# Kernel optimization log

Hardware: AMD Instinct MI355X
Metric: run time of the kernel (lower is better)

## Reference

```python
import jax, jax.numpy as jnp
import numpy as np

N_NODES = 1_000_000
E = 262_144
N_FEAT_COLS = 9        # columns 1..9 of x
CARD = 50_000          # cardinality of each feature embedding table
EMB = 128
EDGE_DIM = 27
# node type (col 0) that activates each feature column h (h = col index - 1):
# files (type 0) use cols 1..4, processes (type 1) use col 5, sockets (type 2) use cols 6..9
TYPE_PER_COL = (0, 0, 0, 0, 1, 2, 2, 2, 2)


def setup_inputs() -> dict:
    key = jax.random.key(0)
    ks = jax.random.split(key, 10)
    type_col = jax.random.randint(ks[0], (N_NODES, 1), 0, 3, dtype=jnp.int32)
    feat_cols = jax.random.randint(ks[1], (N_NODES, N_FEAT_COLS), 0, CARD, dtype=jnp.int32)
    x = jnp.concatenate([type_col, feat_cols], axis=1)  # [N_NODES, 10]
    src = jax.random.randint(ks[2], (E,), 0, N_NODES, dtype=jnp.int32)
    dst = jax.random.randint(ks[3], (E,), 0, N_NODES, dtype=jnp.int32)
    neg_dst = jax.random.randint(ks[4], (E,), 0, N_NODES, dtype=jnp.int32)
    msg = jax.random.normal(ks[5], (E, EDGE_DIM), dtype=jnp.float32)
    emb_type = jax.random.normal(ks[6], (3, EMB), dtype=jnp.float32)            # embeddings[0]
    emb_feats = jax.random.normal(ks[7], (N_FEAT_COLS, CARD, EMB), dtype=jnp.float32)  # embeddings[1..9]
    edge_w = jax.random.normal(ks[8], (EMB, EDGE_DIM), dtype=jnp.float32) / np.sqrt(EDGE_DIM)
    edge_b = jnp.zeros((EMB,), dtype=jnp.float32)
    out_w = jax.random.normal(ks[9], (1, EMB), dtype=jnp.float32) / np.sqrt(EMB)
    out_b = jnp.zeros((1,), dtype=jnp.float32)
    return dict(x=x, src=src, dst=dst, neg_dst=neg_dst, msg=msg,
                emb_type=emb_type, emb_feats=emb_feats,
                edge_w=edge_w, edge_b=edge_b, out_w=out_w, out_b=out_b)


def _encode_features(rows, emb_type, emb_feats):
    """rows: [E,10] int. Equivalent to torch encode_features: per node type,
    sum the type-specific embedding lookups; col-0 (type) embedding is shared."""
    t = rows[:, 0]                     # [E] node type
    out = emb_type[t]                  # embeddings[0] applies to every type
    for h in range(N_FEAT_COLS):       # small fixed loop over 9 tables
        mask = (t == TYPE_PER_COL[h]).astype(out.dtype)[:, None]   # [E,1]
        out = out + emb_feats[h][rows[:, h + 1]] * mask            # masked gather-sum
    return out                         # [E, EMB]


def reference(x, src, dst, neg_dst, msg, emb_type, emb_feats, edge_w, edge_b, out_w, out_b):
    h_src = _encode_features(x[src], emb_type, emb_feats)       # [E, EMB]
    h_pos_dst = _encode_features(x[dst], emb_type, emb_feats)
    h_neg_dst = _encode_features(x[neg_dst], emb_type, emb_feats)
    target_msg = msg @ edge_w.T + edge_b                        # Linear(edge_dim -> EMB)
    h_pos_edge = jax.nn.relu(h_src + h_pos_dst)
    h_neg_edge = jax.nn.relu(h_src + h_neg_dst)
    pos = (h_pos_edge + target_msg) @ out_w.T + out_b           # [E, 1]
    neg = (h_neg_edge + target_msg) @ out_w.T + out_b           # [E, 1]
    return (pos, neg)
```

## Files before the change

### kernel.cpp

```cpp
#include <hip/hip_runtime.h>
#include <hip/hip_fp16.h>

#define N_NODES 1000000
#define NUM_EDGES 262144
#define CARD 50000
#define EMB 128
#define EDGE_DIM 27

typedef float vfloat4 __attribute__((ext_vector_type(4)));
typedef unsigned int vuint4 __attribute__((ext_vector_type(4)));

#define XPACK_OFF 4096
#define EMB16_OFF (XPACK_OFF + (size_t)N_NODES * 16)
#define EMB_ELEMS (9ull * CARD * EMB)
#define WS_NEEDED (EMB16_OFF + EMB_ELEMS * 2)

__global__ void prep_kernel(const float* __restrict__ edge_w,
                            const float* __restrict__ edge_b,
                            const float* __restrict__ out_w,
                            const float* __restrict__ out_b,
                            float* __restrict__ ws) {
    int j = threadIdx.x;
    if (j < EDGE_DIM) {
        float s = 0.f;
        for (int k = 0; k < EMB; ++k) s += out_w[k] * edge_w[k * EDGE_DIM + j];
        ws[j] = s;
    } else if (j == EDGE_DIM) {
        float s = out_b[0];
        for (int k = 0; k < EMB; ++k) s += edge_b[k] * out_w[k];
        ws[EDGE_DIM] = s;
    }
}

__global__ __launch_bounds__(256) void pack_x_kernel(const int* __restrict__ x,
                                                     uint4* __restrict__ xp) {
    int i = blockIdx.x * 256 + threadIdx.x;
    if (i >= N_NODES) return;
    const int* r = x + (size_t)i * 10;
    const int t  = __builtin_nontemporal_load(r + 0);
    const int c1 = __builtin_nontemporal_load(r + 1);
    const int c2 = __builtin_nontemporal_load(r + 2);
    const int c3 = __builtin_nontemporal_load(r + 3);
    const int c4 = __builtin_nontemporal_load(r + 4);
    const int c5 = __builtin_nontemporal_load(r + 5);
    const int c6 = __builtin_nontemporal_load(r + 6);
    const int c7 = __builtin_nontemporal_load(r + 7);
    const int c8 = __builtin_nontemporal_load(r + 8);
    const int c9 = __builtin_nontemporal_load(r + 9);
    unsigned i0, i1, i2, i3, pad = 0;
    if (t == 0) {
        i0 = (unsigned)c1;
        i1 = 1u * CARD + (unsigned)c2;
        i2 = 2u * CARD + (unsigned)c3;
        i3 = 3u * CARD + (unsigned)c4;
    } else if (t == 1) {
        i0 = i1 = i2 = i3 = 4u * CARD + (unsigned)c5;
        pad = 1u;
    } else {
        i0 = 5u * CARD + (unsigned)c6;
        i1 = 6u * CARD + (unsigned)c7;
        i2 = 7u * CARD + (unsigned)c8;
        i3 = 8u * CARD + (unsigned)c9;
    }
    uint4 o;
    o.x = i0 | ((unsigned)t << 20) | (pad << 22);
    o.y = i1;
    o.z = i2;
    o.w = i3;
    xp[i] = o;
}

__global__ __launch_bounds__(256) void cvt_emb_kernel(const float* __restrict__ src,
                                                      __half* __restrict__ dst) {
    size_t i = ((size_t)blockIdx.x * 256 + threadIdx.x) * 8;
    vfloat4 a = __builtin_nontemporal_load((const vfloat4*)(src + i));
    vfloat4 b = __builtin_nontemporal_load((const vfloat4*)(src + i + 4));
    __half2 h0 = __floats2half2_rn(a.x, a.y);
    __half2 h1 = __floats2half2_rn(a.z, a.w);
    __half2 h2 = __floats2half2_rn(b.x, b.y);
    __half2 h3 = __floats2half2_rn(b.z, b.w);
    vuint4 o;
    o.x = *(unsigned*)&h0;
    o.y = *(unsigned*)&h1;
    o.z = *(unsigned*)&h2;
    o.w = *(unsigned*)&h3;
    *(vuint4*)(dst + i) = o;
}

__global__ __launch_bounds__(256, 4) void edge_pred_fp16(
    const uint4* __restrict__ xp, const int* __restrict__ src,
    const int* __restrict__ dst, const int* __restrict__ neg_dst,
    const float* __restrict__ msg, const float* __restrict__ emb_type,
    const __half* __restrict__ e16, const float* __restrict__ out_w,
    const float* __restrict__ ws, float* __restrict__ out) {
    const int lane = threadIdx.x & 63;
    const int wave = threadIdx.x >> 6;
    const int e0 = __builtin_amdgcn_readfirstlane(blockIdx.x * 8 + wave * 2);

    const int half = lane >> 5;
    const int hl = lane & 31;
    const int loff = lane * 2;

    int nodes[6];
    nodes[0] = src[e0];     nodes[1] = dst[e0];     nodes[2] = neg_dst[e0];
    nodes[3] = src[e0 + 1]; nodes[4] = dst[e0 + 1]; nodes[5] = neg_dst[e0 + 1];

    float mterm = 0.f;
    if (hl < EDGE_DIM) {
        mterm = __builtin_nontemporal_load(msg + (size_t)(e0 + half) * EDGE_DIM + hl) * ws[hl];
    }

    float2 v0[6];
    unsigned u[6][4];
    float wpad[6];
#pragma unroll
    for (int n = 0; n < 6; ++n) {
        const uint4 px = xp[nodes[n]];
        const unsigned t = (px.x >> 20) & 3u;
        wpad[n] = (px.x & (1u << 22)) ? 0.f : 1.f;
        const size_t i0 = (size_t)(px.x & 0xFFFFFu);

        v0[n] = *(const float2*)(emb_type + (size_t)t * EMB + loff);
        u[n][0] = *(const unsigned*)((const char*)e16 + (i0 * EMB + loff) * 2);
        u[n][1] = *(const unsigned*)((const char*)e16 + ((size_t)px.y * EMB + loff) * 2);
        u[n][2] = *(const unsigned*)((const char*)e16 + ((size_t)px.z * EMB + loff) * 2);
        u[n][3] = *(const unsigned*)((const char*)e16 + ((size_t)px.w * EMB + loff) * 2);
    }
    const float2 wv = *(const float2*)(out_w + loff);

    __builtin_amdgcn_sched_barrier(0);

    float hx[6], hy[6];
#pragma unroll
    for (int n = 0; n < 6; ++n) {
        const float2 f1 = __half22float2(*(const __half2*)&u[n][0]);
        const float2 f2 = __half22float2(*(const __half2*)&u[n][1]);
        const float2 f3 = __half22float2(*(const __half2*)&u[n][2]);
        const float2 f4 = __half22float2(*(const __half2*)&u[n][3]);
        const float ax = v0[n].x + f1.x;
        const float ay = v0[n].y + f1.y;
        const float bx = f2.x + f3.x + f4.x;
        const float by = f2.y + f3.y + f4.y;
        hx[n] = ax + wpad[n] * bx;
        hy[n] = ay + wpad[n] * by;
    }

    float p0 = fmaxf(hx[0] + hx[1], 0.f) * wv.x + fmaxf(hy[0] + hy[1], 0.f) * wv.y;
    float q0 = fmaxf(hx[0] + hx[2], 0.f) * wv.x + fmaxf(hy[0] + hy[2], 0.f) * wv.y;
    float p1 = fmaxf(hx[3] + hx[4], 0.f) * wv.x + fmaxf(hy[3] + hy[4], 0.f) * wv.y;
    float q1 = fmaxf(hx[3] + hx[5], 0.f) * wv.x + fmaxf(hy[3] + hy[5], 0.f) * wv.y;

    if (half == 0) { p0 += mterm; q0 += mterm; }
    else           { p1 += mterm; q1 += mterm; }

    p0 += __shfl_xor(p0, 32, 64);
    q0 += __shfl_xor(q0, 32, 64);
    p1 += __shfl_xor(p1, 32, 64);
    q1 += __shfl_xor(q1, 32, 64);
    float pz = half ? p1 : p0;
    float qz = half ? q1 : q0;
#pragma unroll
    for (int off = 16; off > 0; off >>= 1) {
        pz += __shfl_xor(pz, off, 64);
        qz += __shfl_xor(qz, off, 64);
    }

    if (hl == 0) {
        const float b2 = ws[EDGE_DIM];
        const int e = e0 + half;
        out[e] = pz + b2;
        out[NUM_EDGES + e] = qz + b2;
    }
}

__global__ __launch_bounds__(256, 4) void edge_pred_kernel(
    const int* __restrict__ x, const int* __restrict__ src,
    const int* __restrict__ dst, const int* __restrict__ neg_dst,
    const float* __restrict__ msg, const float* __restrict__ emb_type,
    const float* __restrict__ emb_feats, const float* __restrict__ out_w,
    const float* __restrict__ ws, float* __restrict__ out) {
    const int lane = threadIdx.x & 63;
    const int wave = threadIdx.x >> 6;
    const int e0 = __builtin_amdgcn_readfirstlane(blockIdx.x * 8 + wave * 2);

    const int half = lane >> 5;
    const int hl = lane & 31;
    const int loff = lane * 2;

    int nodes[6];
    nodes[0] = src[e0];     nodes[1] = dst[e0];     nodes[2] = neg_dst[e0];
    nodes[3] = src[e0 + 1]; nodes[4] = dst[e0 + 1]; nodes[5] = neg_dst[e0 + 1];

    float mterm = 0.f;
    if (hl < EDGE_DIM) {
        mterm = __builtin_nontemporal_load(msg + (size_t)(e0 + half) * EDGE_DIM + hl) * ws[hl];
    }

    float2 v[6][5];
    float wpad[6];
#pragma unroll
    for (int n = 0; n < 6; ++n) {
        const int* xr = x + (size_t)nodes[n] * 10;
        const int t = xr[0];
        const int c1 = xr[1], c2 = xr[2], c3 = xr[3], c4 = xr[4], c5 = xr[5],
                  c6 = xr[6], c7 = xr[7], c8 = xr[8], c9 = xr[9];
        const int i0 = (t == 0) ? c1 : (t == 1) ? c5 : c6;
        const int i1 = (t == 0) ? c2 : (t == 1) ? c5 : c7;
        const int i2 = (t == 0) ? c3 : (t == 1) ? c5 : c8;
        const int i3 = (t == 0) ? c4 : (t == 1) ? c5 : c9;
        const int h0 = (t == 0) ? 0 : (t == 1) ? 4 : 5;
        const int h1 = (t == 0) ? 1 : (t == 1) ? 4 : 6;
        const int h2 = (t == 0) ? 2 : (t == 1) ? 4 : 7;
        const int h3 = (t == 0) ? 3 : (t == 1) ? 4 : 8;
        wpad[n] = (t == 1) ? 0.f : 1.f;

        v[n][0] = *(const float2*)(emb_type + (size_t)t * EMB + loff);
        v[n][1] = *(const float2*)(emb_feats + ((size_t)h0 * CARD + (size_t)i0) * EMB + loff);
        v[n][2] = *(const float2*)(emb_feats + ((size_t)h1 * CARD + (size_t)i1) * EMB + loff);
        v[n][3] = *(const float2*)(emb_feats + ((size_t)h2 * CARD + (size_t)i2) * EMB + loff);
        v[n][4] = *(const float2*)(emb_feats + ((size_t)h3 * CARD + (size_t)i3) * EMB + loff);
    }
    const float2 wv = *(const float2*)(out_w + loff);

    __builtin_amdgcn_sched_barrier(0);

    float hx[6], hy[6];
#pragma unroll
    for (int n = 0; n < 6; ++n) {
        const float ax = v[n][0].x + v[n][1].x;
        const float ay = v[n][0].y + v[n][1].y;
        const float bx = v[n][2].x + v[n][3].x + v[n][4].x;
        const float by = v[n][2].y + v[n][3].y + v[n][4].y;
        hx[n] = ax + wpad[n] * bx;
        hy[n] = ay + wpad[n] * by;
    }

    float p0 = fmaxf(hx[0] + hx[1], 0.f) * wv.x + fmaxf(hy[0] + hy[1], 0.f) * wv.y;
    float q0 = fmaxf(hx[0] + hx[2], 0.f) * wv.x + fmaxf(hy[0] + hy[2], 0.f) * wv.y;
    float p1 = fmaxf(hx[3] + hx[4], 0.f) * wv.x + fmaxf(hy[3] + hy[4], 0.f) * wv.y;
    float q1 = fmaxf(hx[3] + hx[5], 0.f) * wv.x + fmaxf(hy[3] + hy[5], 0.f) * wv.y;

    if (half == 0) { p0 += mterm; q0 += mterm; }
    else           { p1 += mterm; q1 += mterm; }

    p0 += __shfl_xor(p0, 32, 64);
    q0 += __shfl_xor(q0, 32, 64);
    p1 += __shfl_xor(p1, 32, 64);
    q1 += __shfl_xor(q1, 32, 64);
    float pz = half ? p1 : p0;
    float qz = half ? q1 : q0;
#pragma unroll
    for (int off = 16; off > 0; off >>= 1) {
        pz += __shfl_xor(pz, off, 64);
        qz += __shfl_xor(qz, off, 64);
    }

    if (hl == 0) {
        const float b2 = ws[EDGE_DIM];
        const int e = e0 + half;
        out[e] = pz + b2;
        out[NUM_EDGES + e] = qz + b2;
    }
}

extern "C" void kernel_launch(void* const* d_in, const int* in_sizes, int n_in,
                              void* d_out, int out_size, void* d_ws, size_t ws_size,
                              hipStream_t stream) {
    const int* x = (const int*)d_in[0];
    const int* src = (const int*)d_in[1];
    const int* dst = (const int*)d_in[2];
    const int* neg_dst = (const int*)d_in[3];
    const float* msg = (const float*)d_in[4];
    const float* emb_type = (const float*)d_in[5];
    const float* emb_feats = (const float*)d_in[6];
    const float* edge_w = (const float*)d_in[7];
    const float* edge_b = (const float*)d_in[8];
    const float* out_w = (const float*)d_in[9];
    const float* out_b = (const float*)d_in[10];
    float* out = (float*)d_out;
    float* ws = (float*)d_ws;

    prep_kernel<<<1, 64, 0, stream>>>(edge_w, edge_b, out_w, out_b, ws);

    const int blocks = NUM_EDGES / 8;

    if (ws_size >= WS_NEEDED) {
        uint4* xp = (uint4*)((char*)d_ws + XPACK_OFF);
        __half* e16 = (__half*)((char*)d_ws + EMB16_OFF);
        pack_x_kernel<<<(N_NODES + 255) / 256, 256, 0, stream>>>(x, xp);
        cvt_emb_kernel<<<28125, 256, 0, stream>>>(emb_feats, e16);
        edge_pred_fp16<<<blocks, 256, 0, stream>>>(xp, src, dst, neg_dst, msg,
                                                   emb_type, e16, out_w, ws, out);
    } else {
        edge_pred_kernel<<<blocks, 256, 0, stream>>>(x, src, dst, neg_dst, msg,
                                                     emb_type, emb_feats, out_w,
                                                     ws, out);
    }
}
```

Baseline: 473.9 us.

## Merge prep kernels into one launch and process four edges per wave

The separate pack_x and fp16 conversion kernels become a single launch that dispatches on block index, removing one launch and the gap between them. The fp16 edge kernel now handles four edges per wave instead of two, with 12 node gathers in flight per lane and a quarter-wave reduction. This raises memory-level parallelism per wave and halves the grid, at the cost of more registers per thread and possibly lower occupancy.

```diff
diff --git a/kernel.cpp b/kernel.cpp
--- a/kernel.cpp
+++ b/kernel.cpp
@@ -14,6 +14,9 @@
 #define EMB16_OFF (XPACK_OFF + (size_t)N_NODES * 16)
 #define EMB_ELEMS (9ull * CARD * EMB)
 #define WS_NEEDED (EMB16_OFF + EMB_ELEMS * 2)
+
+#define CVT_BLOCKS 28125
+#define PACK_BLOCKS ((N_NODES + 255) / 256)
 
 __global__ void prep_kernel(const float* __restrict__ edge_w,
                             const float* __restrict__ edge_b,
@@ -32,59 +35,59 @@
     }
 }
 
-__global__ __launch_bounds__(256) void pack_x_kernel(const int* __restrict__ x,
-                                                     uint4* __restrict__ xp) {
-    int i = blockIdx.x * 256 + threadIdx.x;
-    if (i >= N_NODES) return;
-    const int* r = x + (size_t)i * 10;
-    const int t  = __builtin_nontemporal_load(r + 0);
-    const int c1 = __builtin_nontemporal_load(r + 1);
-    const int c2 = __builtin_nontemporal_load(r + 2);
-    const int c3 = __builtin_nontemporal_load(r + 3);
-    const int c4 = __builtin_nontemporal_load(r + 4);
-    const int c5 = __builtin_nontemporal_load(r + 5);
-    const int c6 = __builtin_nontemporal_load(r + 6);
-    const int c7 = __builtin_nontemporal_load(r + 7);
-    const int c8 = __builtin_nontemporal_load(r + 8);
-    const int c9 = __builtin_nontemporal_load(r + 9);
-    unsigned i0, i1, i2, i3, pad = 0;
-    if (t == 0) {
-        i0 = (unsigned)c1;
-        i1 = 1u * CARD + (unsigned)c2;
-        i2 = 2u * CARD + (unsigned)c3;
-        i3 = 3u * CARD + (unsigned)c4;
-    } else if (t == 1) {
-        i0 = i1 = i2 = i3 = 4u * CARD + (unsigned)c5;
-        pad = 1u;
+__global__ __launch_bounds__(256) void prep_stream_kernel(
+    const float* __restrict__ embf, __half* __restrict__ dst,
+    const int* __restrict__ x, uint4* __restrict__ xp) {
+    if (blockIdx.x < CVT_BLOCKS) {
+        size_t i = ((size_t)blockIdx.x * 256 + threadIdx.x) * 8;
+        vfloat4 a = __builtin_nontemporal_load((const vfloat4*)(embf + i));
+        vfloat4 b = __builtin_nontemporal_load((const vfloat4*)(embf + i + 4));
+        __half2 h0 = __floats2half2_rn(a.x, a.y);
+        __half2 h1 = __floats2half2_rn(a.z, a.w);
+        __half2 h2 = __floats2half2_rn(b.x, b.y);
+        __half2 h3 = __floats2half2_rn(b.z, b.w);
+        vuint4 o;
+        o.x = *(unsigned*)&h0;
+        o.y = *(unsigned*)&h1;
+        o.z = *(unsigned*)&h2;
+        o.w = *(unsigned*)&h3;
+        *(vuint4*)(dst + i) = o;
     } else {
-        i0 = 5u * CARD + (unsigned)c6;
-        i1 = 6u * CARD + (unsigned)c7;
-        i2 = 7u * CARD + (unsigned)c8;
-        i3 = 8u * CARD + (unsigned)c9;
-    }
-    uint4 o;
-    o.x = i0 | ((unsigned)t << 20) | (pad << 22);
-    o.y = i1;
-    o.z = i2;
-    o.w = i3;
-    xp[i] = o;
-}
-
-__global__ __launch_bounds__(256) void cvt_emb_kernel(const float* __restrict__ src,
-                                                      __half* __restrict__ dst) {
-    size_t i = ((size_t)blockIdx.x * 256 + threadIdx.x) * 8;
-    vfloat4 a = __builtin_nontemporal_load((const vfloat4*)(src + i));
-    vfloat4 b = __builtin_nontemporal_load((const vfloat4*)(src + i + 4));
-    __half2 h0 = __floats2half2_rn(a.x, a.y);
-    __half2 h1 = __floats2half2_rn(a.z, a.w);
-    __half2 h2 = __floats2half2_rn(b.x, b.y);
-    __half2 h3 = __floats2half2_rn(b.z, b.w);
-    vuint4 o;
-    o.x = *(unsigned*)&h0;
-    o.y = *(unsigned*)&h1;
-    o.z = *(unsigned*)&h2;
-    o.w = *(unsigned*)&h3;
-    *(vuint4*)(dst + i) = o;
+        int i = (blockIdx.x - CVT_BLOCKS) * 256 + threadIdx.x;
+        if (i >= N_NODES) return;
+        const int* r = x + (size_t)i * 10;
+        const int t  = __builtin_nontemporal_load(r + 0);
+        const int c1 = __builtin_nontemporal_load(r + 1);
+        const int c2 = __builtin_nontemporal_load(r + 2);
+        const int c3 = __builtin_nontemporal_load(r + 3);
+        const int c4 = __builtin_nontemporal_load(r + 4);
+        const int c5 = __builtin_nontemporal_load(r + 5);
+        const int c6 = __builtin_nontemporal_load(r + 6);
+        const int c7 = __builtin_nontemporal_load(r + 7);
+        const int c8 = __builtin_nontemporal_load(r + 8);
+        const int c9 = __builtin_nontemporal_load(r + 9);
+        unsigned i0, i1, i2, i3, pad = 0;
+        if (t == 0) {
+            i0 = (unsigned)c1;
+            i1 = 1u * CARD + (unsigned)c2;
+            i2 = 2u * CARD + (unsigned)c3;
+            i3 = 3u * CARD + (unsigned)c4;
+        } else if (t == 1) {
+            i0 = i1 = i2 = i3 = 4u * CARD + (unsigned)c5;
+            pad = 1u;
+        } else {
+            i0 = 5u * CARD + (unsigned)c6;
+            i1 = 6u * CARD + (unsigned)c7;
+            i2 = 7u * CARD + (unsigned)c8;
+            i3 = 8u * CARD + (unsigned)c9;
+        }
+        uint4 o;
+        o.x = i0 | ((unsigned)t << 20) | (pad << 22);
+        o.y = i1;
+        o.z = i2;
+        o.w = i3;
+        xp[i] = o;
+    }
 }
 
 __global__ __launch_bounds__(256, 4) void edge_pred_fp16(
@@ -95,26 +98,34 @@
     const float* __restrict__ ws, float* __restrict__ out) {
     const int lane = threadIdx.x & 63;
     const int wave = threadIdx.x >> 6;
-    const int e0 = __builtin_amdgcn_readfirstlane(blockIdx.x * 8 + wave * 2);
-
-    const int half = lane >> 5;
-    const int hl = lane & 31;
+    const int e0 = __builtin_amdgcn_readfirstlane(blockIdx.x * 16 + wave * 4);
+
+    const int q = lane >> 4;
+    const int ql = lane & 15;
     const int loff = lane * 2;
 
-    int nodes[6];
-    nodes[0] = src[e0];     nodes[1] = dst[e0];     nodes[2] = neg_dst[e0];
-    nodes[3] = src[e0 + 1]; nodes[4] = dst[e0 + 1]; nodes[5] = neg_dst[e0 + 1];
-
-    float mterm = 0.f;
-    if (hl < EDGE_DIM) {
-        mterm = __builtin_nontemporal_load(msg + (size_t)(e0 + half) * EDGE_DIM + hl) * ws[hl];
-    }
-
-    float2 v0[6];
-    unsigned u[6][4];
-    float wpad[6];
-#pragma unroll
-    for (int n = 0; n < 6; ++n) {
+    int nodes[12];
+#pragma unroll
+    for (int k = 0; k < 4; ++k) {
+        nodes[3 * k + 0] = src[e0 + k];
+        nodes[3 * k + 1] = dst[e0 + k];
+        nodes[3 * k + 2] = neg_dst[e0 + k];
+    }
+
+    float mterm;
+    {
+        const float* mrow = msg + (size_t)(e0 + q) * EDGE_DIM;
+        mterm = __builtin_nontemporal_load(mrow + ql) * ws[ql];
+        if (ql < EDGE_DIM - 16) {
+            mterm += __builtin_nontemporal_load(mrow + 16 + ql) * ws[16 + ql];
+        }
+    }
+
+    float2 v0[12];
+    unsigned u[12][4];
+    float wpad[12];
+#pragma unroll
+    for (int n = 0; n < 12; ++n) {
         const uint4 px = xp[nodes[n]];
         const unsigned t = (px.x >> 20) & 3u;
         wpad[n] = (px.x & (1u << 22)) ? 0.f : 1.f;
@@ -130,9 +141,9 @@
 
     __builtin_amdgcn_sched_barrier(0);
 
-    float hx[6], hy[6];
-#pragma unroll
-    for (int n = 0; n < 6; ++n) {
+    float hx[12], hy[12];
+#pragma unroll
+    for (int n = 0; n < 12; ++n) {
         const float2 f1 = __half22float2(*(const __half2*)&u[n][0]);
         const float2 f2 = __half22float2(*(const __half2*)&u[n][1]);
         const float2 f3 = __half22float2(*(const __half2*)&u[n][2]);
@@ -145,31 +156,45 @@
         hy[n] = ay + wpad[n] * by;
     }
 
-    float p0 = fmaxf(hx[0] + hx[1], 0.f) * wv.x + fmaxf(hy[0] + hy[1], 0.f) * wv.y;
-    float q0 = fmaxf(hx[0] + hx[2], 0.f) * wv.x + fmaxf(hy[0] + hy[2], 0.f) * wv.y;
-    float p1 = fmaxf(hx[3] + hx[4], 0.f) * wv.x + fmaxf(hy[3] + hy[4], 0.f) * wv.y;
-    float q1 = fmaxf(hx[3] + hx[5], 0.f) * wv.x + fmaxf(hy[3] + hy[5], 0.f) * wv.y;
-
-    if (half == 0) { p0 += mterm; q0 += mterm; }
-    else           { p1 += mterm; q1 += mterm; }
-
-    p0 += __shfl_xor(p0, 32, 64);
-    q0 += __shfl_xor(q0, 32, 64);
-    p1 += __shfl_xor(p1, 32, 64);
-    q1 += __shfl_xor(q1, 32, 64);
-    float pz = half ? p1 : p0;
-    float qz = half ? q1 : q0;
-#pragma unroll
-    for (int off = 16; off > 0; off >>= 1) {
-        pz += __shfl_xor(pz, off, 64);
-        qz += __shfl_xor(qz, off, 64);
-    }
-
-    if (hl == 0) {
+    float p0, p1, p2, p3, q0, q1, q2, q3;
+    {
+        p0 = fmaxf(hx[0] + hx[1], 0.f) * wv.x + fmaxf(hy[0] + hy[1], 0.f) * wv.y;
+        q0 = fmaxf(hx[0] + hx[2], 0.f) * wv.x + fmaxf(hy[0] + hy[2], 0.f) * wv.y;
+        p1 = fmaxf(hx[3] + hx[4], 0.f) * wv.x + fmaxf(hy[3] + hy[4], 0.f) * wv.y;
+        q1 = fmaxf(hx[3] + hx[5], 0.f) * wv.x + fmaxf(hy[3] + hy[5], 0.f) * wv.y;
+        p2 = fmaxf(hx[6] + hx[7], 0.f) * wv.x + fmaxf(hy[6] + hy[7], 0.f) * wv.y;
+        q2 = fmaxf(hx[6] + hx[8], 0.f) * wv.x + fmaxf(hy[6] + hy[8], 0.f) * wv.y;
+        p3 = fmaxf(hx[9] + hx[10], 0.f) * wv.x + fmaxf(hy[9] + hy[10], 0.f) * wv.y;
+        q3 = fmaxf(hx[9] + hx[11], 0.f) * wv.x + fmaxf(hy[9] + hy[11], 0.f) * wv.y;
+    }
+
+    if (q == 0) { p0 += mterm; q0 += mterm; }
+    else if (q == 1) { p1 += mterm; q1 += mterm; }
+    else if (q == 2) { p2 += mterm; q2 += mterm; }
+    else             { p3 += mterm; q3 += mterm; }
+
+    p0 += __shfl_xor(p0, 32, 64); p0 += __shfl_xor(p0, 16, 64);
+    q0 += __shfl_xor(q0, 32, 64); q0 += __shfl_xor(q0, 16, 64);
+    p1 += __shfl_xor(p1, 32, 64); p1 += __shfl_xor(p1, 16, 64);
+    q1 += __shfl_xor(q1, 32, 64); q1 += __shfl_xor(q1, 16, 64);
+    p2 += __shfl_xor(p2, 32, 64); p2 += __shfl_xor(p2, 16, 64);
+    q2 += __shfl_xor(q2, 32, 64); q2 += __shfl_xor(q2, 16, 64);
+    p3 += __shfl_xor(p3, 32, 64); p3 += __shfl_xor(p3, 16, 64);
+    q3 += __shfl_xor(q3, 32, 64); q3 += __shfl_xor(q3, 16, 64);
+
+    float zp = (q == 0) ? p0 : (q == 1) ? p1 : (q == 2) ? p2 : p3;
+    float zq = (q == 0) ? q0 : (q == 1) ? q1 : (q == 2) ? q2 : q3;
+#pragma unroll
+    for (int off = 8; off > 0; off >>= 1) {
+        zp += __shfl_xor(zp, off, 64);
+        zq += __shfl_xor(zq, off, 64);
+    }
+
+    if (ql == 0) {
         const float b2 = ws[EDGE_DIM];
-        const int e = e0 + half;
-        out[e] = pz + b2;
-        out[NUM_EDGES + e] = qz + b2;
+        const int e = e0 + q;
+        out[e] = zp + b2;
+        out[NUM_EDGES + e] = zq + b2;
     }
 }
 
@@ -282,16 +307,16 @@
 
     prep_kernel<<<1, 64, 0, stream>>>(edge_w, edge_b, out_w, out_b, ws);
 
-    const int blocks = NUM_EDGES / 8;
-
     if (ws_size >= WS_NEEDED) {
         uint4* xp = (uint4*)((char*)d_ws + XPACK_OFF);
         __half* e16 = (__half*)((char*)d_ws + EMB16_OFF);
-        pack_x_kernel<<<(N_NODES + 255) / 256, 256, 0, stream>>>(x, xp);
-        cvt_emb_kernel<<<28125, 256, 0, stream>>>(emb_feats, e16);
+        prep_stream_kernel<<<CVT_BLOCKS + PACK_BLOCKS, 256, 0, stream>>>(
+            emb_feats, e16, x, xp);
+        const int blocks = NUM_EDGES / 16;
         edge_pred_fp16<<<blocks, 256, 0, stream>>>(xp, src, dst, neg_dst, msg,
                                                    emb_type, e16, out_w, ws, out);
     } else {
+        const int blocks = NUM_EDGES / 8;
         edge_pred_kernel<<<blocks, 256, 0, stream>>>(x, src, dst, neg_dst, msg,
                                                      emb_type, emb_feats, out_w,
                                                      ws, out);
```

Result: slower. 484.9 us (+2.3%).

## Merge prep kernels into one streaming launch and precompute per-edge message term

Applied to the files above, without the earlier changes.

Combines the embedding fp16 conversion and node-index packing into a single kernel launch, partitioned by block index. A third block range computes the per-edge message dot product into a workspace array. The main gather kernel then reads one precomputed float per edge instead of loading msg rows, and writes outputs with nontemporal stores. This removes one launch boundary and takes the strided msg loads off the gather kernel, at the cost of an extra small workspace array and a dependency on ws from prep_kernel.

```diff
diff --git a/kernel.cpp b/kernel.cpp
--- a/kernel.cpp
+++ b/kernel.cpp
@@ -10,10 +10,15 @@
 typedef float vfloat4 __attribute__((ext_vector_type(4)));
 typedef unsigned int vuint4 __attribute__((ext_vector_type(4)));
 
-#define XPACK_OFF 4096
+#define MTERM_OFF 4096
+#define XPACK_OFF (MTERM_OFF + (size_t)NUM_EDGES * 4)
 #define EMB16_OFF (XPACK_OFF + (size_t)N_NODES * 16)
 #define EMB_ELEMS (9ull * CARD * EMB)
 #define WS_NEEDED (EMB16_OFF + EMB_ELEMS * 2)
+
+#define CVT_BLOCKS 28125
+#define PACK_BLOCKS ((N_NODES + 255) / 256)
+#define MSG_BLOCKS (NUM_EDGES / 256)
 
 __global__ void prep_kernel(const float* __restrict__ edge_w,
                             const float* __restrict__ edge_b,
@@ -32,67 +37,78 @@
     }
 }
 
-__global__ __launch_bounds__(256) void pack_x_kernel(const int* __restrict__ x,
-                                                     uint4* __restrict__ xp) {
-    int i = blockIdx.x * 256 + threadIdx.x;
-    if (i >= N_NODES) return;
-    const int* r = x + (size_t)i * 10;
-    const int t  = __builtin_nontemporal_load(r + 0);
-    const int c1 = __builtin_nontemporal_load(r + 1);
-    const int c2 = __builtin_nontemporal_load(r + 2);
-    const int c3 = __builtin_nontemporal_load(r + 3);
-    const int c4 = __builtin_nontemporal_load(r + 4);
-    const int c5 = __builtin_nontemporal_load(r + 5);
-    const int c6 = __builtin_nontemporal_load(r + 6);
-    const int c7 = __builtin_nontemporal_load(r + 7);
-    const int c8 = __builtin_nontemporal_load(r + 8);
-    const int c9 = __builtin_nontemporal_load(r + 9);
-    unsigned i0, i1, i2, i3, pad = 0;
-    if (t == 0) {
-        i0 = (unsigned)c1;
-        i1 = 1u * CARD + (unsigned)c2;
-        i2 = 2u * CARD + (unsigned)c3;
-        i3 = 3u * CARD + (unsigned)c4;
-    } else if (t == 1) {
-        i0 = i1 = i2 = i3 = 4u * CARD + (unsigned)c5;
-        pad = 1u;
+__global__ __launch_bounds__(256) void prep_stream_kernel(
+    const float* __restrict__ embf, __half* __restrict__ dst,
+    const int* __restrict__ x, uint4* __restrict__ xp,
+    const float* __restrict__ msg, const float* __restrict__ ws,
+    float* __restrict__ mterm) {
+    if (blockIdx.x < CVT_BLOCKS) {
+        size_t i = ((size_t)blockIdx.x * 256 + threadIdx.x) * 8;
+        vfloat4 a = __builtin_nontemporal_load((const vfloat4*)(embf + i));
+        vfloat4 b = __builtin_nontemporal_load((const vfloat4*)(embf + i + 4));
+        __half2 h0 = __floats2half2_rn(a.x, a.y);
+        __half2 h1 = __floats2half2_rn(a.z, a.w);
+        __half2 h2 = __floats2half2_rn(b.x, b.y);
+        __half2 h3 = __floats2half2_rn(b.z, b.w);
+        vuint4 o;
+        o.x = *(unsigned*)&h0;
+        o.y = *(unsigned*)&h1;
+        o.z = *(unsigned*)&h2;
+        o.w = *(unsigned*)&h3;
+        *(vuint4*)(dst + i) = o;
+    } else if (blockIdx.x < CVT_BLOCKS + PACK_BLOCKS) {
+        int i = (blockIdx.x - CVT_BLOCKS) * 256 + threadIdx.x;
+        if (i >= N_NODES) return;
+        const int* r = x + (size_t)i * 10;
+        const int t  = __builtin_nontemporal_load(r + 0);
+        const int c1 = __builtin_nontemporal_load(r + 1);
+        const int c2 = __builtin_nontemporal_load(r + 2);
+        const int c3 = __builtin_nontemporal_load(r + 3);
+        const int c4 = __builtin_nontemporal_load(r + 4);
+        const int c5 = __builtin_nontemporal_load(r + 5);
+        const int c6 = __builtin_nontemporal_load(r + 6);
+        const int c7 = __builtin_nontemporal_load(r + 7);
+        const int c8 = __builtin_nontemporal_load(r + 8);
+        const int c9 = __builtin_nontemporal_load(r + 9);
+        unsigned i0, i1, i2, i3, pad = 0;
+        if (t == 0) {
+            i0 = (unsigned)c1;
+            i1 = 1u * CARD + (unsigned)c2;
+            i2 = 2u * CARD + (unsigned)c3;
+            i3 = 3u * CARD + (unsigned)c4;
+        } else if (t == 1) {
+            i0 = i1 = i2 = i3 = 4u * CARD + (unsigned)c5;
+            pad = 1u;
+        } else {
+            i0 = 5u * CARD + (unsigned)c6;
+            i1 = 6u * CARD + (unsigned)c7;
+            i2 = 7u * CARD + (unsigned)c8;
+            i3 = 8u * CARD + (unsigned)c9;
+        }
+        uint4 o;
+        o.x = i0 | ((unsigned)t << 20) | (pad << 22);
+        o.y = i1;
+        o.z = i2;
+        o.w = i3;
+        xp[i] = o;
     } else {
-        i0 = 5u * CARD + (unsigned)c6;
-        i1 = 6u * CARD + (unsigned)c7;
-        i2 = 7u * CARD + (unsigned)c8;
-        i3 = 8u * CARD + (unsigned)c9;
-    }
-    uint4 o;
-    o.x = i0 | ((unsigned)t << 20) | (pad << 22);
-    o.y = i1;
-    o.z = i2;
-    o.w = i3;
-    xp[i] = o;
-}
-
-__global__ __launch_bounds__(256) void cvt_emb_kernel(const float* __restrict__ src,
-                                                      __half* __restrict__ dst) {
-    size_t i = ((size_t)blockIdx.x * 256 + threadIdx.x) * 8;
-    vfloat4 a = __builtin_nontemporal_load((const vfloat4*)(src + i));
-    vfloat4 b = __builtin_nontemporal_load((const vfloat4*)(src + i + 4));
-    __half2 h0 = __floats2half2_rn(a.x, a.y);
-    __half2 h1 = __floats2half2_rn(a.z, a.w);
-    __half2 h2 = __floats2half2_rn(b.x, b.y);
-    __half2 h3 = __floats2half2_rn(b.z, b.w);
-    vuint4 o;
-    o.x = *(unsigned*)&h0;
-    o.y = *(unsigned*)&h1;
-    o.z = *(unsigned*)&h2;
-    o.w = *(unsigned*)&h3;
-    *(vuint4*)(dst + i) = o;
+        int e = (blockIdx.x - CVT_BLOCKS - PACK_BLOCKS) * 256 + threadIdx.x;
+        const float* mrow = msg + (size_t)e * EDGE_DIM;
+        float s = 0.f;
+#pragma unroll
+        for (int j = 0; j < EDGE_DIM; ++j) {
+            s += __builtin_nontemporal_load(mrow + j) * ws[j];
+        }
+        mterm[e] = s;
+    }
 }
 
 __global__ __launch_bounds__(256, 4) void edge_pred_fp16(
     const uint4* __restrict__ xp, const int* __restrict__ src,
     const int* __restrict__ dst, const int* __restrict__ neg_dst,
-    const float* __restrict__ msg, const float* __restrict__ emb_type,
-    const __half* __restrict__ e16, const float* __restrict__ out_w,
-    const float* __restrict__ ws, float* __restrict__ out) {
+    const float* __restrict__ emb_type, const __half* __restrict__ e16,
+    const float* __restrict__ out_w, const float* __restrict__ ws,
+    const float* __restrict__ mterm, float* __restrict__ out) {
     const int lane = threadIdx.x & 63;
     const int wave = threadIdx.x >> 6;
     const int e0 = __builtin_amdgcn_readfirstlane(blockIdx.x * 8 + wave * 2);
@@ -104,11 +120,8 @@
     int nodes[6];
     nodes[0] = src[e0];     nodes[1] = dst[e0];     nodes[2] = neg_dst[e0];
     nodes[3] = src[e0 + 1]; nodes[4] = dst[e0 + 1]; nodes[5] = neg_dst[e0 + 1];
-
-    float mterm = 0.f;
-    if (hl < EDGE_DIM) {
-        mterm = __builtin_nontemporal_load(msg + (size_t)(e0 + half) * EDGE_DIM + hl) * ws[hl];
-    }
+    const float mt0 = mterm[e0];
+    const float mt1 = mterm[e0 + 1];
 
     float2 v0[6];
     unsigned u[6][4];
@@ -150,9 +163,6 @@
     float p1 = fmaxf(hx[3] + hx[4], 0.f) * wv.x + fmaxf(hy[3] + hy[4], 0.f) * wv.y;
     float q1 = fmaxf(hx[3] + hx[5], 0.f) * wv.x + fmaxf(hy[3] + hy[5], 0.f) * wv.y;
 
-    if (half == 0) { p0 += mterm; q0 += mterm; }
-    else           { p1 += mterm; q1 += mterm; }
-
     p0 += __shfl_xor(p0, 32, 64);
     q0 += __shfl_xor(q0, 32, 64);
     p1 += __shfl_xor(p1, 32, 64);
@@ -166,10 +176,10 @@
     }
 
     if (hl == 0) {
-        const float b2 = ws[EDGE_DIM];
+        const float bm = ws[EDGE_DIM] + (half ? mt1 : mt0);
         const int e = e0 + half;
-        out[e] = pz + b2;
-        out[NUM_EDGES + e] = qz + b2;
+        __builtin_nontemporal_store(pz + bm, out + e);
+        __builtin_nontemporal_store(qz + bm, out + NUM_EDGES + e);
     }
 }
 
@@ -282,16 +292,18 @@
 
     prep_kernel<<<1, 64, 0, stream>>>(edge_w, edge_b, out_w, out_b, ws);
 
-    const int blocks = NUM_EDGES / 8;
-
     if (ws_size >= WS_NEEDED) {
+        float* mterm = (float*)((char*)d_ws + MTERM_OFF);
         uint4* xp = (uint4*)((char*)d_ws + XPACK_OFF);
         __half* e16 = (__half*)((char*)d_ws + EMB16_OFF);
-        pack_x_kernel<<<(N_NODES + 255) / 256, 256, 0, stream>>>(x, xp);
-        cvt_emb_kernel<<<28125, 256, 0, stream>>>(emb_feats, e16);
-        edge_pred_fp16<<<blocks, 256, 0, stream>>>(xp, src, dst, neg_dst, msg,
-                                                   emb_type, e16, out_w, ws, out);
+        prep_stream_kernel<<<CVT_BLOCKS + PACK_BLOCKS + MSG_BLOCKS, 256, 0,
+                             stream>>>(emb_feats, e16, x, xp, msg, ws, mterm);
+        const int blocks = NUM_EDGES / 8;
+        edge_pred_fp16<<<blocks, 256, 0, stream>>>(xp, src, dst, neg_dst,
+                                                   emb_type, e16, out_w, ws,
+                                                   mterm, out);
     } else {
+        const int blocks = NUM_EDGES / 8;
         edge_pred_kernel<<<blocks, 256, 0, stream>>>(x, src, dst, neg_dst, msg,
                                                      emb_type, emb_feats, out_w,
                                                      ws, out);
```

Result: slower. 487.6 us (+2.9%).
